# Kernel optimization log

Measured on AMD Instinct MI355X. Metric: run time of the kernel, lower is better.

The kernel has to match this reference:

```python
import jax, jax.numpy as jnp
import numpy as np

B, S, D, H, M = 2, 2048, 1024, 16, 4096  # batch, seqlen, dim, n_heads, max_seq_len
HD = D // H  # head_dim = 64
EPS = 1e-5


def layernorm(x, g, b):
    mu = jnp.mean(x, axis=-1, keepdims=True)
    var = jnp.mean((x - mu) ** 2, axis=-1, keepdims=True)
    return (x - mu) * jax.lax.rsqrt(var + EPS) * g + b


def setup_inputs() -> dict:
    key = jax.random.key(0)
    ks = jax.random.split(key, 5)
    x = jax.random.normal(ks[0], (B, S, D), jnp.float32)
    # causal mask: >=0 -> keep, negative -> drop (forward does att *= mask >= 0)
    i = jnp.arange(S)
    mask = jnp.where(i[None, :] <= i[:, None], 0, -1).astype(jnp.int32)[None, None]
    w1 = jax.random.normal(ks[1], (4 * D, D), jnp.float32) * (D ** -0.5)
    b1 = jnp.zeros((4 * D,), jnp.float32)
    w2 = jax.random.normal(ks[2], (D, D), jnp.float32) * (D ** -0.5)
    b2 = jnp.zeros((D,), jnp.float32)
    g1 = jnp.ones((D,), jnp.float32)
    beta1 = jnp.zeros((D,), jnp.float32)
    g2 = jnp.ones((D,), jnp.float32)
    beta2 = jnp.zeros((D,), jnp.float32)
    pos_w = jax.random.normal(ks[3], (2 * M - 1,), jnp.float32) * 0.02
    return dict(x=x, mask=mask, w1=w1, b1=b1, w2=w2, b2=b2,
                g1=g1, beta1=beta1, g2=g2, beta2=beta2, pos_w=pos_w)


def reference(x, mask, w1, b1, w2, b2, g1, beta1, g2, beta2, pos_w):
    # f1 + silu, split into gate u and q/k/v
    h = jax.nn.silu(x @ w1.T + b1)                      # [B,S,4D]
    u, q, k, v = jnp.split(h, 4, axis=-1)
    to_heads = lambda t: t.reshape(B, S, H, HD).transpose(0, 2, 1, 3)  # [B,H,S,HD]
    u, q, k, v = map(to_heads, (u, q, k, v))
    # relative positional bias: bias[i,j] = pos_w[M-1 + (j - i)]
    rel = jnp.arange(S)[None, :] - jnp.arange(S)[:, None]
    bias = pos_w[M - 1 + rel]                           # [S,S]
    att = jax.nn.silu(jnp.einsum('bhqd,bhkd->bhqk', q, k) + bias)
    att = att * (mask >= 0)                             # [B,H,S,S]
    y = jnp.einsum('bhqk,bhkd->bhqd', att, v) * u
    y = y.transpose(0, 2, 1, 3).reshape(B, S, D)
    y = layernorm(y, g1, beta1)
    y = y @ w2.T + b2
    return layernorm(y + x, g2, beta2)
```

## Files before the change

### kernel.cpp

```cpp
#include <hip/hip_runtime.h>
#include <hip/hip_bf16.h>

#define BN   2
#define SEQ  2048
#define DIM  1024
#define NH   16
#define HD   64
#define D4   4096
#define MAXS 4096

using bf16 = __hip_bfloat16;
typedef __bf16 bf16x8 __attribute__((ext_vector_type(8)));
typedef float  f32x4  __attribute__((ext_vector_type(4)));

__device__ __forceinline__ float bf2f(bf16 v){ return __bfloat162float(v); }
__device__ __forceinline__ bf16  f2bf(float v){ return __float2bfloat16(v); }
__device__ __forceinline__ float silu_f(float v){
  const float e = __expf(-v);
  return v * __builtin_amdgcn_rcpf(1.f + e);
}

__device__ __forceinline__ void async16(void* lds, const void* g){
  __builtin_amdgcn_global_load_lds((const __attribute__((address_space(1))) void*)g,
                                   (__attribute__((address_space(3))) void*)lds, 16, 0, 0);
}
__device__ __forceinline__ f32x4 mfma16(bf16x8 a, bf16x8 b, f32x4 c){
  return __builtin_amdgcn_mfma_f32_16x16x32_bf16(a, b, c, 0, 0, 0);
}

__global__ __launch_bounds__(256) void f2bk3(
    const float* __restrict__ a, bf16* __restrict__ ao, int na,
    const float* __restrict__ b, bf16* __restrict__ bo, int nb,
    const float* __restrict__ c, bf16* __restrict__ co)
{
  int i = (blockIdx.x * 256 + threadIdx.x) * 4;
  const float* in; bf16* out;
  if (i < na){ in = a; out = ao; }
  else if (i < na + nb){ in = b; out = bo; i -= na; }
  else { in = c; out = co; i -= na + nb; }
  const float4 v = *(const float4*)(in + i);
  bf16 t0 = f2bf(v.x), t1 = f2bf(v.y), t2 = f2bf(v.z), t3 = f2bf(v.w);
  ushort4 o;
  o.x = *(unsigned short*)&t0; o.y = *(unsigned short*)&t1;
  o.z = *(unsigned short*)&t2; o.w = *(unsigned short*)&t3;
  *(ushort4*)((unsigned short*)out + i) = o;
}

template<int NTOT>
__global__ __launch_bounds__(256) void gemm_bt(
    const bf16* __restrict__ A, const bf16* __restrict__ W,
    const float* __restrict__ bias, bf16* __restrict__ outb, bf16* __restrict__ vt)
{
  constexpr int K = DIM;
  const int ntiles = NTOT / 128;
  const int m0 = (int)(blockIdx.x / ntiles) * 128;
  const int n0 = (int)(blockIdx.x % ntiles) * 128;
  __shared__ bf16 Al[128*32];
  __shared__ bf16 Bl[128*32];
  const int tid = threadIdx.x, wave = tid>>6, lane = tid&63;
  const int quad = lane>>4, l16 = lane&15;
  const int srow = lane>>2;
  const int sg   = ((lane&3) ^ ((lane>>3)&3)) * 8;
  const int wm = (wave>>1)*64, wn = (wave&1)*64;
  const int rkey = ((l16>>1)&3);

  f32x4 acc[4][4];
  #pragma unroll
  for (int i=0;i<4;i++)
    #pragma unroll
    for (int j=0;j<4;j++) acc[i][j] = (f32x4){0.f,0.f,0.f,0.f};

  const bf16* aB = A + m0*K;
  const bf16* wB = W + n0*K;

  for (int k0 = 0; k0 < K; k0 += 32){
    async16(&Al[wave*1024      ], aB + (wave*32      + srow)*K + k0 + sg);
    async16(&Al[wave*1024 + 512], aB + (wave*32 + 16 + srow)*K + k0 + sg);
    async16(&Bl[wave*1024      ], wB + (wave*32      + srow)*K + k0 + sg);
    async16(&Bl[wave*1024 + 512], wB + (wave*32 + 16 + srow)*K + k0 + sg);
    __syncthreads();
    bf16x8 af[4], bv[4];
    #pragma unroll
    for (int mt=0;mt<4;mt++) af[mt] = *(const bf16x8*)&Al[(wm+mt*16+l16)*32 + (quad ^ rkey)*8];
    #pragma unroll
    for (int nt=0;nt<4;nt++) bv[nt] = *(const bf16x8*)&Bl[(wn+nt*16+l16)*32 + (quad ^ rkey)*8];
    #pragma unroll
    for (int mt=0;mt<4;mt++)
      #pragma unroll
      for (int nt=0;nt<4;nt++)
        acc[mt][nt] = mfma16(af[mt], bv[nt], acc[mt][nt]);
    __syncthreads();
  }

  const bool vtile = (NTOT == 4096) && (n0 >= 3*DIM);
  if (!vtile){
    #pragma unroll
    for (int mt=0;mt<4;mt++){
      #pragma unroll
      for (int nt=0;nt<4;nt++){
        const int row = m0 + wm + mt*16 + quad*4;
        const int col = n0 + wn + nt*16 + l16;
        const float bvv = bias[col];
        #pragma unroll
        for (int r=0;r<4;r++){
          float v = silu_f(acc[mt][nt][r] + bvv);
          outb[(row+r)*NTOT + col] = f2bf(v);
        }
      }
    }
  } else {
    #pragma unroll
    for (int mt=0;mt<4;mt++){
      #pragma unroll
      for (int nt=0;nt<4;nt++){
        const int row = m0 + wm + mt*16 + quad*4;
        const int colg = n0 + wn + nt*16 + l16;
        const float bvv = bias[colg];
        const int col = colg - 3*DIM;
        const int hh = col >> 6, d = col & 63;
        const int bb = row >> 11, sl = row & 2047;
        ushort4 o;
        float v0 = silu_f(acc[mt][nt][0] + bvv);
        float v1 = silu_f(acc[mt][nt][1] + bvv);
        float v2 = silu_f(acc[mt][nt][2] + bvv);
        float v3 = silu_f(acc[mt][nt][3] + bvv);
        bf16 t0=f2bf(v0), t1=f2bf(v1), t2=f2bf(v2), t3=f2bf(v3);
        o.x=*(unsigned short*)&t0; o.y=*(unsigned short*)&t1;
        o.z=*(unsigned short*)&t2; o.w=*(unsigned short*)&t3;
        *(ushort4*)&vt[((bb*NH + hh)*HD + d)*SEQ + sl] = o;
      }
    }
  }
}

__global__ __launch_bounds__(256) void gemm_bt2(
    const bf16* __restrict__ A, const bf16* __restrict__ W,
    const float* __restrict__ bias, const float* __restrict__ resid,
    float* __restrict__ outf)
{
  constexpr int K = DIM, NTOT = DIM;
  const int ntiles = NTOT / 64;
  const int m0 = (int)(blockIdx.x / ntiles) * 128;
  const int n0 = (int)(blockIdx.x % ntiles) * 64;
  __shared__ bf16 Al[128*32];
  __shared__ bf16 Bl[64*32];
  const int tid = threadIdx.x, wave = tid>>6, lane = tid&63;
  const int quad = lane>>4, l16 = lane&15;
  const int srow = lane>>2;
  const int sg   = ((lane&3) ^ ((lane>>3)&3)) * 8;
  const int wm = wave*32;
  const int rkey = ((l16>>1)&3);

  f32x4 acc[2][4];
  #pragma unroll
  for (int i=0;i<2;i++)
    #pragma unroll
    for (int j=0;j<4;j++) acc[i][j] = (f32x4){0.f,0.f,0.f,0.f};

  const bf16* aB = A + m0*K;
  const bf16* wB = W + n0*K;

  for (int k0 = 0; k0 < K; k0 += 32){
    async16(&Al[wave*1024      ], aB + (wave*32      + srow)*K + k0 + sg);
    async16(&Al[wave*1024 + 512], aB + (wave*32 + 16 + srow)*K + k0 + sg);
    async16(&Bl[wave*512       ], wB + (wave*16      + srow)*K + k0 + sg);
    __syncthreads();
    bf16x8 af[2], bv[4];
    #pragma unroll
    for (int mt=0;mt<2;mt++) af[mt] = *(const bf16x8*)&Al[(wm+mt*16+l16)*32 + (quad ^ rkey)*8];
    #pragma unroll
    for (int nt=0;nt<4;nt++) bv[nt] = *(const bf16x8*)&Bl[(nt*16+l16)*32 + (quad ^ rkey)*8];
    #pragma unroll
    for (int mt=0;mt<2;mt++)
      #pragma unroll
      for (int nt=0;nt<4;nt++)
        acc[mt][nt] = mfma16(af[mt], bv[nt], acc[mt][nt]);
    __syncthreads();
  }

  #pragma unroll
  for (int mt=0;mt<2;mt++){
    #pragma unroll
    for (int nt=0;nt<4;nt++){
      const int row = m0 + wm + mt*16 + quad*4;
      const int col = n0 + nt*16 + l16;
      const float bvv = bias[col];
      #pragma unroll
      for (int r=0;r<4;r++){
        outf[(row+r)*NTOT + col] = acc[mt][nt][r] + bvv + resid[(row+r)*NTOT + col];
      }
    }
  }
}

__global__ __launch_bounds__(256) void attn(
    const bf16* __restrict__ h, const bf16* __restrict__ vt,
    const float* __restrict__ pw, bf16* __restrict__ y)
{
  const int bid = blockIdx.x;
  const int g  = (bid & 7) + ((bid >> 7) << 3);
  const int qp = (bid >> 3) & 15;
  const int hh = g & 15, b = g >> 4;
  __shared__ bf16 Kl[128*64];
  __shared__ bf16 Vl[64*128];
  __shared__ bf16 Pl[4][16*136];
  __shared__ float pwl[256];
  const int tid = threadIdx.x, wave = tid>>6, lane = tid&63;
  const int quad = lane>>4, l16 = lane&15;

  const bf16* kgb = h + b*SEQ*D4 + 2*DIM + hh*HD;
  const bf16* vgb = vt + (b*NH + hh)*HD*SEQ;
  const int krow8 = lane>>3;
  const int kgo   = ((lane&7) ^ krow8) * 8;
  const int vrow4 = lane>>4;

  #pragma unroll
  for (int pass = 0; pass < 2; ++pass){
    const int qt = pass ? (31 - qp) : qp;
    const int q0 = qt * 64;

    const bf16* qbase = h + (b*SEQ + q0 + wave*16 + l16)*D4 + DIM + hh*HD;
    bf16x8 qf[2];
    qf[0] = *(const bf16x8*)(qbase + quad*8);
    qf[1] = *(const bf16x8*)(qbase + 32 + quad*8);

    f32x4 oacc[4];
    #pragma unroll
    for (int nt=0;nt<4;nt++) oacc[nt] = (f32x4){0.f,0.f,0.f,0.f};

    const int kmax = q0 + 64;
    for (int k0 = 0; k0 < kmax; k0 += 128){
      #pragma unroll
      for (int t=0;t<4;t++)
        async16(&Kl[(wave*32 + t*8)*64], kgb + (k0 + wave*32 + t*8 + krow8)*D4 + kgo);
      #pragma unroll
      for (int t=0;t<4;t++){
        const int vg = ((lane&15) ^ (t*4 + vrow4)) * 8;
        async16(&Vl[(wave*16 + t*4)*128], vgb + (wave*16 + t*4 + vrow4)*SEQ + k0 + vg);
      }
      const int W0 = MAXS - 1 + k0 - q0 - 63;
      if (wave == 0) async16(&pwl[0], pw + W0 + lane*4);
      __syncthreads();

      f32x4 sacc[8];
      #pragma unroll
      for (int nt=0;nt<8;nt++) sacc[nt] = (f32x4){0.f,0.f,0.f,0.f};
      #pragma unroll
      for (int ks=0;ks<2;ks++){
        #pragma unroll
        for (int nt=0;nt<8;nt++){
          bf16x8 kf = *(const bf16x8*)&Kl[(nt*16 + l16)*64 + ((ks*4 + quad) ^ (l16&7))*8];
          sacc[nt] = mfma16(kf, qf[ks], sacc[nt]);
        }
      }

      const int dq = q0 - k0;
      const int qrl = wave*16 + l16;
      #pragma unroll
      for (int nt=0;nt<8;nt++){
        const int kb = nt*16 + quad*4;
        const int d0 = kb - qrl;
        ushort4 o;
        bf16 tb[4];
        #pragma unroll
        for (int r=0;r<4;r++){
          const int d = kb + r - qrl;
          const float bias = pwl[d + 63];
          const float sv = silu_f(sacc[nt][r] + bias);
          tb[r] = f2bf((d <= dq) ? sv : 0.f);
        }
        (void)d0;
        o.x=*(unsigned short*)&tb[0]; o.y=*(unsigned short*)&tb[1];
        o.z=*(unsigned short*)&tb[2]; o.w=*(unsigned short*)&tb[3];
        *(ushort4*)&Pl[wave][l16*136 + kb] = o;
      }

      #pragma unroll
      for (int ks=0;ks<4;ks++){
        bf16x8 pf = *(const bf16x8*)&Pl[wave][l16*136 + ks*32 + quad*8];
        #pragma unroll
        for (int nt=0;nt<4;nt++){
          bf16x8 vf = *(const bf16x8*)&Vl[(nt*16 + l16)*128 + ((ks*4 + quad) ^ l16)*8];
          oacc[nt] = mfma16(pf, vf, oacc[nt]);
        }
      }
      __syncthreads();
    }

    const int qrow = q0 + wave*16 + quad*4;
    #pragma unroll
    for (int nt=0;nt<4;nt++){
      const int c = hh*HD + nt*16 + l16;
      #pragma unroll
      for (int r=0;r<4;r++){
        const int srow = b*SEQ + qrow + r;
        const float uu = bf2f(h[srow*D4 + c]);
        y[srow*DIM + c] = f2bf(oacc[nt][r] * uu);
      }
    }
    __syncthreads();
  }
}


template<bool FP32IN, bool FP32OUT>
__global__ __launch_bounds__(256) void lnorm(const void* __restrict__ in,
    const float* __restrict__ g, const float* __restrict__ be, void* __restrict__ out)
{
  const int row = blockIdx.x;
  const int tid = threadIdx.x, wave = tid>>6, lane = tid&63;
  const int c0 = tid*4;
  float v[4];
  if (FP32IN){
    const float* p = (const float*)in + row*DIM + c0;
    #pragma unroll
    for (int j=0;j<4;j++) v[j] = p[j];
  } else {
    const bf16* p = (const bf16*)in + row*DIM + c0;
    #pragma unroll
    for (int j=0;j<4;j++) v[j] = bf2f(p[j]);
  }
  float s = 0.f, ss = 0.f;
  #pragma unroll
  for (int j=0;j<4;j++){ s += v[j]; ss += v[j]*v[j]; }
  #pragma unroll
  for (int off=32; off>0; off>>=1){
    s  += __shfl_down(s, off);
    ss += __shfl_down(ss, off);
  }
  __shared__ float red[8];
  if (lane==0){ red[wave] = s; red[4+wave] = ss; }
  __syncthreads();
  s  = red[0]+red[1]+red[2]+red[3];
  ss = red[4]+red[5]+red[6]+red[7];
  const float mu   = s * (1.f/DIM);
  const float var  = ss * (1.f/DIM) - mu*mu;
  const float rstd = rsqrtf(var + 1e-5f);
  #pragma unroll
  for (int j=0;j<4;j++){
    const int c = c0 + j;
    const float o = (v[j]-mu)*rstd*g[c] + be[c];
    if (FP32OUT) ((float*)out)[row*DIM + c] = o;
    else         ((bf16*)out)[row*DIM + c] = f2bf(o);
  }
}

extern "C" void kernel_launch(void* const* d_in, const int* in_sizes, int n_in,
                              void* d_out, int out_size, void* d_ws, size_t ws_size,
                              hipStream_t stream)
{
  const float* x   = (const float*)d_in[0];
  const float* w1  = (const float*)d_in[2];
  const float* b1  = (const float*)d_in[3];
  const float* w2  = (const float*)d_in[4];
  const float* b2  = (const float*)d_in[5];
  const float* g1  = (const float*)d_in[6];
  const float* be1 = (const float*)d_in[7];
  const float* g2  = (const float*)d_in[8];
  const float* be2 = (const float*)d_in[9];
  const float* pw  = (const float*)d_in[10];

  char* ws = (char*)d_ws;
  bf16*  h   = (bf16*)(ws);
  bf16*  vt  = (bf16*)(ws + (32u<<20));
  bf16*  y   = (bf16*)(ws + (40u<<20));
  bf16*  xb  = (bf16*)(ws + (48u<<20));
  bf16*  w1b = (bf16*)(ws + (56u<<20));
  bf16*  w2b = (bf16*)(ws + (64u<<20));
  bf16*  l1  = (bf16*)(ws + (66u<<20));
  float* z   = (float*)(ws + (74u<<20));

  const int NX  = BN*SEQ*DIM;
  const int NW1 = 4*DIM*DIM;
  const int NW2 = DIM*DIM;
  f2bk3<<<dim3((NX+NW1+NW2)/1024), dim3(256), 0, stream>>>(x, xb, NX, w1, w1b, NW1, w2, w2b);

  gemm_bt<4096><<<dim3(1024), dim3(256), 0, stream>>>(xb, w1b, b1, h, vt);
  attn<<<dim3(512), dim3(256), 0, stream>>>(h, vt, pw, y);
  lnorm<false,false><<<dim3(4096), dim3(256), 0, stream>>>(y, g1, be1, l1);
  gemm_bt2<<<dim3(512), dim3(256), 0, stream>>>(l1, w2b, b2, x, z);
  lnorm<true,true><<<dim3(4096), dim3(256), 0, stream>>>(z, g2, be2, d_out);
}
```

Baseline: 244.3 us.

## Split attention KV range across two blocks and fuse u-gating into layernorm

The attention grid doubles. Each block now handles alternating 64-key chunks (an even/odd split) and writes fp32 partial outputs to two buffers, where before one block ran 128-key chunks. A new layernorm kernel sums the two partials, multiplies by the u gate and normalizes, which moves the gating out of the attention epilogue. This gives more parallelism and smaller LDS tiles for better occupancy. In exchange it writes and reads two fp32 partial arrays, adds extra global traffic and reuses workspace regions.

```diff
diff --git a/kernel.cpp b/kernel.cpp
--- a/kernel.cpp
+++ b/kernel.cpp
@@ -195,28 +195,34 @@
 
 __global__ __launch_bounds__(256) void attn(
     const bf16* __restrict__ h, const bf16* __restrict__ vt,
-    const float* __restrict__ pw, bf16* __restrict__ y)
-{
-  const int bid = blockIdx.x;
-  const int g  = (bid & 7) + ((bid >> 7) << 3);
-  const int qp = (bid >> 3) & 15;
+    const float* __restrict__ pw, float* __restrict__ yp0, float* __restrict__ yp1)
+{
+  const int bid  = blockIdx.x;
+  const int xcd  = bid & 7;
+  const int idx  = bid >> 3;
+  const int g    = ((idx >> 5) << 3) | xcd;
+  const int slot = idx & 31;
+  const int p    = slot >> 1;
+  const int ksp  = slot & 1;
   const int hh = g & 15, b = g >> 4;
-  __shared__ bf16 Kl[128*64];
-  __shared__ bf16 Vl[64*128];
-  __shared__ bf16 Pl[4][16*136];
+  float* __restrict__ yp = ksp ? yp1 : yp0;
+
+  __shared__ bf16 Kl[64*64];
+  __shared__ bf16 Vl[64*64];
+  __shared__ bf16 Pl[4][16*72];
   __shared__ float pwl[256];
+
   const int tid = threadIdx.x, wave = tid>>6, lane = tid&63;
   const int quad = lane>>4, l16 = lane&15;
+  const int r8 = lane>>3;
+  const int g8 = ((lane&7) ^ r8) * 8;
 
   const bf16* kgb = h + b*SEQ*D4 + 2*DIM + hh*HD;
   const bf16* vgb = vt + (b*NH + hh)*HD*SEQ;
-  const int krow8 = lane>>3;
-  const int kgo   = ((lane&7) ^ krow8) * 8;
-  const int vrow4 = lane>>4;
 
   #pragma unroll
   for (int pass = 0; pass < 2; ++pass){
-    const int qt = pass ? (31 - qp) : qp;
+    const int qt = pass ? (31 - p) : p;
     const int q0 = qt * 64;
 
     const bf16* qbase = h + (b*SEQ + q0 + wave*16 + l16)*D4 + DIM + hh*HD;
@@ -228,27 +234,24 @@
     #pragma unroll
     for (int nt=0;nt<4;nt++) oacc[nt] = (f32x4){0.f,0.f,0.f,0.f};
 
-    const int kmax = q0 + 64;
-    for (int k0 = 0; k0 < kmax; k0 += 128){
-      #pragma unroll
-      for (int t=0;t<4;t++)
-        async16(&Kl[(wave*32 + t*8)*64], kgb + (k0 + wave*32 + t*8 + krow8)*D4 + kgo);
-      #pragma unroll
-      for (int t=0;t<4;t++){
-        const int vg = ((lane&15) ^ (t*4 + vrow4)) * 8;
-        async16(&Vl[(wave*16 + t*4)*128], vgb + (wave*16 + t*4 + vrow4)*SEQ + k0 + vg);
-      }
-      const int W0 = MAXS - 1 + k0 - q0 - 63;
-      if (wave == 0) async16(&pwl[0], pw + W0 + lane*4);
+    for (int ic = ksp; ic <= qt; ic += 2){
+      const int k0 = ic * 64;
+      #pragma unroll
+      for (int t=0;t<2;t++)
+        async16(&Kl[(wave*16 + t*8)*64], kgb + (k0 + wave*16 + t*8 + r8)*D4 + g8);
+      #pragma unroll
+      for (int t=0;t<2;t++)
+        async16(&Vl[(wave*16 + t*8)*64], vgb + (wave*16 + t*8 + r8)*SEQ + k0 + g8);
+      if (wave == 0) async16(&pwl[0], pw + (MAXS-1 + k0 - q0 - 63) + lane*4);
       __syncthreads();
 
-      f32x4 sacc[8];
-      #pragma unroll
-      for (int nt=0;nt<8;nt++) sacc[nt] = (f32x4){0.f,0.f,0.f,0.f};
+      f32x4 sacc[4];
+      #pragma unroll
+      for (int nt=0;nt<4;nt++) sacc[nt] = (f32x4){0.f,0.f,0.f,0.f};
       #pragma unroll
       for (int ks=0;ks<2;ks++){
         #pragma unroll
-        for (int nt=0;nt<8;nt++){
+        for (int nt=0;nt<4;nt++){
           bf16x8 kf = *(const bf16x8*)&Kl[(nt*16 + l16)*64 + ((ks*4 + quad) ^ (l16&7))*8];
           sacc[nt] = mfma16(kf, qf[ks], sacc[nt]);
         }
@@ -257,10 +260,8 @@
       const int dq = q0 - k0;
       const int qrl = wave*16 + l16;
       #pragma unroll
-      for (int nt=0;nt<8;nt++){
+      for (int nt=0;nt<4;nt++){
         const int kb = nt*16 + quad*4;
-        const int d0 = kb - qrl;
-        ushort4 o;
         bf16 tb[4];
         #pragma unroll
         for (int r=0;r<4;r++){
@@ -269,18 +270,18 @@
           const float sv = silu_f(sacc[nt][r] + bias);
           tb[r] = f2bf((d <= dq) ? sv : 0.f);
         }
-        (void)d0;
+        ushort4 o;
         o.x=*(unsigned short*)&tb[0]; o.y=*(unsigned short*)&tb[1];
         o.z=*(unsigned short*)&tb[2]; o.w=*(unsigned short*)&tb[3];
-        *(ushort4*)&Pl[wave][l16*136 + kb] = o;
-      }
-
-      #pragma unroll
-      for (int ks=0;ks<4;ks++){
-        bf16x8 pf = *(const bf16x8*)&Pl[wave][l16*136 + ks*32 + quad*8];
+        *(ushort4*)&Pl[wave][l16*72 + kb] = o;
+      }
+
+      #pragma unroll
+      for (int ks=0;ks<2;ks++){
+        bf16x8 pf = *(const bf16x8*)&Pl[wave][l16*72 + ks*32 + quad*8];
         #pragma unroll
         for (int nt=0;nt<4;nt++){
-          bf16x8 vf = *(const bf16x8*)&Vl[(nt*16 + l16)*128 + ((ks*4 + quad) ^ l16)*8];
+          bf16x8 vf = *(const bf16x8*)&Vl[(nt*16 + l16)*64 + ((ks*4 + quad) ^ (l16&7))*8];
           oacc[nt] = mfma16(pf, vf, oacc[nt]);
         }
       }
@@ -293,32 +294,32 @@
       const int c = hh*HD + nt*16 + l16;
       #pragma unroll
       for (int r=0;r<4;r++){
-        const int srow = b*SEQ + qrow + r;
-        const float uu = bf2f(h[srow*D4 + c]);
-        y[srow*DIM + c] = f2bf(oacc[nt][r] * uu);
+        yp[(b*SEQ + qrow + r)*DIM + c] = oacc[nt][r];
       }
     }
-    __syncthreads();
-  }
-}
-
-
-template<bool FP32IN, bool FP32OUT>
-__global__ __launch_bounds__(256) void lnorm(const void* __restrict__ in,
-    const float* __restrict__ g, const float* __restrict__ be, void* __restrict__ out)
+  }
+}
+
+__global__ __launch_bounds__(256) void lnorm_fuse(
+    const float* __restrict__ ya, const float* __restrict__ yb,
+    const bf16* __restrict__ h, const float* __restrict__ g,
+    const float* __restrict__ be, bf16* __restrict__ out)
 {
   const int row = blockIdx.x;
   const int tid = threadIdx.x, wave = tid>>6, lane = tid&63;
   const int c0 = tid*4;
+  const float4 a  = *(const float4*)(ya + row*DIM + c0);
+  const float4 bb = *(const float4*)(yb + row*DIM + c0);
+  const ushort4 uu = *(const ushort4*)((const unsigned short*)h + row*D4 + c0);
   float v[4];
-  if (FP32IN){
-    const float* p = (const float*)in + row*DIM + c0;
-    #pragma unroll
-    for (int j=0;j<4;j++) v[j] = p[j];
-  } else {
-    const bf16* p = (const bf16*)in + row*DIM + c0;
-    #pragma unroll
-    for (int j=0;j<4;j++) v[j] = bf2f(p[j]);
+  {
+    bf16 u0,u1,u2,u3;
+    *(unsigned short*)&u0 = uu.x; *(unsigned short*)&u1 = uu.y;
+    *(unsigned short*)&u2 = uu.z; *(unsigned short*)&u3 = uu.w;
+    v[0] = (a.x + bb.x) * bf2f(u0);
+    v[1] = (a.y + bb.y) * bf2f(u1);
+    v[2] = (a.z + bb.z) * bf2f(u2);
+    v[3] = (a.w + bb.w) * bf2f(u3);
   }
   float s = 0.f, ss = 0.f;
   #pragma unroll
@@ -339,9 +340,38 @@
   #pragma unroll
   for (int j=0;j<4;j++){
     const int c = c0 + j;
-    const float o = (v[j]-mu)*rstd*g[c] + be[c];
-    if (FP32OUT) ((float*)out)[row*DIM + c] = o;
-    else         ((bf16*)out)[row*DIM + c] = f2bf(o);
+    out[row*DIM + c] = f2bf((v[j]-mu)*rstd*g[c] + be[c]);
+  }
+}
+
+__global__ __launch_bounds__(256) void lnorm2k(const float* __restrict__ in,
+    const float* __restrict__ g, const float* __restrict__ be, float* __restrict__ out)
+{
+  const int row = blockIdx.x;
+  const int tid = threadIdx.x, wave = tid>>6, lane = tid&63;
+  const int c0 = tid*4;
+  const float4 a = *(const float4*)(in + row*DIM + c0);
+  float v[4] = {a.x, a.y, a.z, a.w};
+  float s = 0.f, ss = 0.f;
+  #pragma unroll
+  for (int j=0;j<4;j++){ s += v[j]; ss += v[j]*v[j]; }
+  #pragma unroll
+  for (int off=32; off>0; off>>=1){
+    s  += __shfl_down(s, off);
+    ss += __shfl_down(ss, off);
+  }
+  __shared__ float red[8];
+  if (lane==0){ red[wave] = s; red[4+wave] = ss; }
+  __syncthreads();
+  s  = red[0]+red[1]+red[2]+red[3];
+  ss = red[4]+red[5]+red[6]+red[7];
+  const float mu   = s * (1.f/DIM);
+  const float var  = ss * (1.f/DIM) - mu*mu;
+  const float rstd = rsqrtf(var + 1e-5f);
+  #pragma unroll
+  for (int j=0;j<4;j++){
+    const int c = c0 + j;
+    out[row*DIM + c] = (v[j]-mu)*rstd*g[c] + be[c];
   }
 }
 
@@ -363,12 +393,13 @@
   char* ws = (char*)d_ws;
   bf16*  h   = (bf16*)(ws);
   bf16*  vt  = (bf16*)(ws + (32u<<20));
-  bf16*  y   = (bf16*)(ws + (40u<<20));
-  bf16*  xb  = (bf16*)(ws + (48u<<20));
-  bf16*  w1b = (bf16*)(ws + (56u<<20));
-  bf16*  w2b = (bf16*)(ws + (64u<<20));
-  bf16*  l1  = (bf16*)(ws + (66u<<20));
-  float* z   = (float*)(ws + (74u<<20));
+  float* y0  = (float*)(ws + (40u<<20));
+  float* y1  = (float*)(ws + (56u<<20));
+  bf16*  xb  = (bf16*)(ws + (72u<<20));
+  bf16*  w1b = (bf16*)(ws + (80u<<20));
+  bf16*  w2b = (bf16*)(ws + (88u<<20));
+  bf16*  l1  = (bf16*)(ws + (32u<<20));
+  float* z   = (float*)(ws + (40u<<20));
 
   const int NX  = BN*SEQ*DIM;
   const int NW1 = 4*DIM*DIM;
@@ -376,8 +407,8 @@
   f2bk3<<<dim3((NX+NW1+NW2)/1024), dim3(256), 0, stream>>>(x, xb, NX, w1, w1b, NW1, w2, w2b);
 
   gemm_bt<4096><<<dim3(1024), dim3(256), 0, stream>>>(xb, w1b, b1, h, vt);
-  attn<<<dim3(512), dim3(256), 0, stream>>>(h, vt, pw, y);
-  lnorm<false,false><<<dim3(4096), dim3(256), 0, stream>>>(y, g1, be1, l1);
+  attn<<<dim3(1024), dim3(256), 0, stream>>>(h, vt, pw, y0, y1);
+  lnorm_fuse<<<dim3(4096), dim3(256), 0, stream>>>(y0, y1, h, g1, be1, l1);
   gemm_bt2<<<dim3(512), dim3(256), 0, stream>>>(l1, w2b, b2, x, z);
-  lnorm<true,true><<<dim3(4096), dim3(256), 0, stream>>>(z, g2, be2, d_out);
-}
+  lnorm2k<<<dim3(4096), dim3(256), 0, stream>>>(z, g2, be2, (float*)d_out);
+}
```

New measurement: 246.2 us. About the same (+0.8%).

## Double GEMM K-step, swap MFMA operands for vector epilogues, split V projection

Applied to the files above, without the earlier changes.

Both GEMMs now stage 64-wide K slices in LDS with an 8-way XOR swizzle, halving the number of barrier pairs per tile. The first GEMM is split into two kernels: one for u/q/k with transposed MFMA operands so each lane writes four contiguous bf16 outputs with a float4 bias load, and one for the transposed V store. The second GEMM uses the same operand swap to get float4 residual loads and stores. The attention score MFMA operands are also swapped, which changes the P write into LDS to scalar stores. The cost is larger LDS footprint per block and an extra kernel launch.

```diff
diff --git a/kernel.cpp b/kernel.cpp
--- a/kernel.cpp
+++ b/kernel.cpp
@@ -46,23 +46,20 @@
   *(ushort4*)((unsigned short*)out + i) = o;
 }
 
-template<int NTOT>
-__global__ __launch_bounds__(256) void gemm_bt(
+__global__ __launch_bounds__(256) void gemm1_ct(
     const bf16* __restrict__ A, const bf16* __restrict__ W,
-    const float* __restrict__ bias, bf16* __restrict__ outb, bf16* __restrict__ vt)
+    const float* __restrict__ bias, bf16* __restrict__ outb)
 {
   constexpr int K = DIM;
-  const int ntiles = NTOT / 128;
-  const int m0 = (int)(blockIdx.x / ntiles) * 128;
-  const int n0 = (int)(blockIdx.x % ntiles) * 128;
-  __shared__ bf16 Al[128*32];
-  __shared__ bf16 Bl[128*32];
+  const int m0 = (int)(blockIdx.x / 24) * 128;
+  const int n0 = (int)(blockIdx.x % 24) * 128;
+  __shared__ bf16 Al[128*64];
+  __shared__ bf16 Bl[128*64];
   const int tid = threadIdx.x, wave = tid>>6, lane = tid&63;
   const int quad = lane>>4, l16 = lane&15;
-  const int srow = lane>>2;
-  const int sg   = ((lane&3) ^ ((lane>>3)&3)) * 8;
   const int wm = (wave>>1)*64, wn = (wave&1)*64;
-  const int rkey = ((l16>>1)&3);
+  const int srow = wave*8 + (lane>>3);
+  const int sg   = ((lane&7) ^ ((lane>>3)&7)) * 8;
 
   f32x4 acc[4][4];
   #pragma unroll
@@ -73,122 +70,180 @@
   const bf16* aB = A + m0*K;
   const bf16* wB = W + n0*K;
 
-  for (int k0 = 0; k0 < K; k0 += 32){
-    async16(&Al[wave*1024      ], aB + (wave*32      + srow)*K + k0 + sg);
-    async16(&Al[wave*1024 + 512], aB + (wave*32 + 16 + srow)*K + k0 + sg);
-    async16(&Bl[wave*1024      ], wB + (wave*32      + srow)*K + k0 + sg);
-    async16(&Bl[wave*1024 + 512], wB + (wave*32 + 16 + srow)*K + k0 + sg);
-    __syncthreads();
-    bf16x8 af[4], bv[4];
-    #pragma unroll
-    for (int mt=0;mt<4;mt++) af[mt] = *(const bf16x8*)&Al[(wm+mt*16+l16)*32 + (quad ^ rkey)*8];
-    #pragma unroll
-    for (int nt=0;nt<4;nt++) bv[nt] = *(const bf16x8*)&Bl[(wn+nt*16+l16)*32 + (quad ^ rkey)*8];
-    #pragma unroll
-    for (int mt=0;mt<4;mt++)
+  for (int k0 = 0; k0 < K; k0 += 64){
+    #pragma unroll
+    for (int s=0;s<4;s++){
+      async16(&Al[(s*32 + wave*8)*64], aB + (s*32 + srow)*K + k0 + sg);
+      async16(&Bl[(s*32 + wave*8)*64], wB + (s*32 + srow)*K + k0 + sg);
+    }
+    __syncthreads();
+    #pragma unroll
+    for (int ks=0;ks<2;ks++){
+      bf16x8 af[4], bv[4];
+      #pragma unroll
+      for (int mt=0;mt<4;mt++) af[mt] = *(const bf16x8*)&Al[(wm+mt*16+l16)*64 + ((ks*4+quad) ^ (l16&7))*8];
+      #pragma unroll
+      for (int nt=0;nt<4;nt++) bv[nt] = *(const bf16x8*)&Bl[(wn+nt*16+l16)*64 + ((ks*4+quad) ^ (l16&7))*8];
       #pragma unroll
       for (int nt=0;nt<4;nt++)
-        acc[mt][nt] = mfma16(af[mt], bv[nt], acc[mt][nt]);
-    __syncthreads();
-  }
-
-  const bool vtile = (NTOT == 4096) && (n0 >= 3*DIM);
-  if (!vtile){
+        #pragma unroll
+        for (int mt=0;mt<4;mt++)
+          acc[nt][mt] = mfma16(bv[nt], af[mt], acc[nt][mt]);
+    }
+    __syncthreads();
+  }
+
+  #pragma unroll
+  for (int nt=0;nt<4;nt++){
+    const int n = n0 + wn + nt*16 + quad*4;
+    const float4 b4 = *(const float4*)&bias[n];
     #pragma unroll
     for (int mt=0;mt<4;mt++){
-      #pragma unroll
-      for (int nt=0;nt<4;nt++){
-        const int row = m0 + wm + mt*16 + quad*4;
-        const int col = n0 + wn + nt*16 + l16;
-        const float bvv = bias[col];
-        #pragma unroll
-        for (int r=0;r<4;r++){
-          float v = silu_f(acc[mt][nt][r] + bvv);
-          outb[(row+r)*NTOT + col] = f2bf(v);
-        }
-      }
-    }
-  } else {
-    #pragma unroll
-    for (int mt=0;mt<4;mt++){
-      #pragma unroll
-      for (int nt=0;nt<4;nt++){
-        const int row = m0 + wm + mt*16 + quad*4;
-        const int colg = n0 + wn + nt*16 + l16;
-        const float bvv = bias[colg];
-        const int col = colg - 3*DIM;
-        const int hh = col >> 6, d = col & 63;
-        const int bb = row >> 11, sl = row & 2047;
-        ushort4 o;
-        float v0 = silu_f(acc[mt][nt][0] + bvv);
-        float v1 = silu_f(acc[mt][nt][1] + bvv);
-        float v2 = silu_f(acc[mt][nt][2] + bvv);
-        float v3 = silu_f(acc[mt][nt][3] + bvv);
-        bf16 t0=f2bf(v0), t1=f2bf(v1), t2=f2bf(v2), t3=f2bf(v3);
-        o.x=*(unsigned short*)&t0; o.y=*(unsigned short*)&t1;
-        o.z=*(unsigned short*)&t2; o.w=*(unsigned short*)&t3;
-        *(ushort4*)&vt[((bb*NH + hh)*HD + d)*SEQ + sl] = o;
-      }
-    }
-  }
-}
-
-__global__ __launch_bounds__(256) void gemm_bt2(
+      const int m = m0 + wm + mt*16 + l16;
+      bf16 t0 = f2bf(silu_f(acc[nt][mt][0] + b4.x));
+      bf16 t1 = f2bf(silu_f(acc[nt][mt][1] + b4.y));
+      bf16 t2 = f2bf(silu_f(acc[nt][mt][2] + b4.z));
+      bf16 t3 = f2bf(silu_f(acc[nt][mt][3] + b4.w));
+      ushort4 o;
+      o.x=*(unsigned short*)&t0; o.y=*(unsigned short*)&t1;
+      o.z=*(unsigned short*)&t2; o.w=*(unsigned short*)&t3;
+      *(ushort4*)&outb[m*D4 + n] = o;
+    }
+  }
+}
+
+__global__ __launch_bounds__(256) void gemm1_v(
+    const bf16* __restrict__ A, const bf16* __restrict__ W,
+    const float* __restrict__ bias, bf16* __restrict__ vt)
+{
+  constexpr int K = DIM;
+  const int m0 = (int)(blockIdx.x >> 3) * 128;
+  const int n0 = 3*DIM + (int)(blockIdx.x & 7) * 128;
+  __shared__ bf16 Al[128*64];
+  __shared__ bf16 Bl[128*64];
+  const int tid = threadIdx.x, wave = tid>>6, lane = tid&63;
+  const int quad = lane>>4, l16 = lane&15;
+  const int wm = (wave>>1)*64, wn = (wave&1)*64;
+  const int srow = wave*8 + (lane>>3);
+  const int sg   = ((lane&7) ^ ((lane>>3)&7)) * 8;
+
+  f32x4 acc[4][4];
+  #pragma unroll
+  for (int i=0;i<4;i++)
+    #pragma unroll
+    for (int j=0;j<4;j++) acc[i][j] = (f32x4){0.f,0.f,0.f,0.f};
+
+  const bf16* aB = A + m0*K;
+  const bf16* wB = W + n0*K;
+
+  for (int k0 = 0; k0 < K; k0 += 64){
+    #pragma unroll
+    for (int s=0;s<4;s++){
+      async16(&Al[(s*32 + wave*8)*64], aB + (s*32 + srow)*K + k0 + sg);
+      async16(&Bl[(s*32 + wave*8)*64], wB + (s*32 + srow)*K + k0 + sg);
+    }
+    __syncthreads();
+    #pragma unroll
+    for (int ks=0;ks<2;ks++){
+      bf16x8 af[4], bv[4];
+      #pragma unroll
+      for (int mt=0;mt<4;mt++) af[mt] = *(const bf16x8*)&Al[(wm+mt*16+l16)*64 + ((ks*4+quad) ^ (l16&7))*8];
+      #pragma unroll
+      for (int nt=0;nt<4;nt++) bv[nt] = *(const bf16x8*)&Bl[(wn+nt*16+l16)*64 + ((ks*4+quad) ^ (l16&7))*8];
+      #pragma unroll
+      for (int mt=0;mt<4;mt++)
+        #pragma unroll
+        for (int nt=0;nt<4;nt++)
+          acc[mt][nt] = mfma16(af[mt], bv[nt], acc[mt][nt]);
+    }
+    __syncthreads();
+  }
+
+  #pragma unroll
+  for (int mt=0;mt<4;mt++){
+    #pragma unroll
+    for (int nt=0;nt<4;nt++){
+      const int row = m0 + wm + mt*16 + quad*4;
+      const int colg = n0 + wn + nt*16 + l16;
+      const float bvv = bias[colg];
+      const int col = colg - 3*DIM;
+      const int hh = col >> 6, d = col & 63;
+      const int bb = row >> 11, sl = row & 2047;
+      float v0 = silu_f(acc[mt][nt][0] + bvv);
+      float v1 = silu_f(acc[mt][nt][1] + bvv);
+      float v2 = silu_f(acc[mt][nt][2] + bvv);
+      float v3 = silu_f(acc[mt][nt][3] + bvv);
+      bf16 t0=f2bf(v0), t1=f2bf(v1), t2=f2bf(v2), t3=f2bf(v3);
+      ushort4 o;
+      o.x=*(unsigned short*)&t0; o.y=*(unsigned short*)&t1;
+      o.z=*(unsigned short*)&t2; o.w=*(unsigned short*)&t3;
+      *(ushort4*)&vt[((bb*NH + hh)*HD + d)*SEQ + sl] = o;
+    }
+  }
+}
+
+__global__ __launch_bounds__(256) void gemm2_ct(
     const bf16* __restrict__ A, const bf16* __restrict__ W,
     const float* __restrict__ bias, const float* __restrict__ resid,
     float* __restrict__ outf)
 {
   constexpr int K = DIM, NTOT = DIM;
-  const int ntiles = NTOT / 64;
-  const int m0 = (int)(blockIdx.x / ntiles) * 128;
-  const int n0 = (int)(blockIdx.x % ntiles) * 64;
-  __shared__ bf16 Al[128*32];
-  __shared__ bf16 Bl[64*32];
+  const int m0 = (int)(blockIdx.x >> 4) * 128;
+  const int n0 = (int)(blockIdx.x & 15) * 64;
+  __shared__ bf16 Al[128*64];
+  __shared__ bf16 Bl[64*64];
   const int tid = threadIdx.x, wave = tid>>6, lane = tid&63;
   const int quad = lane>>4, l16 = lane&15;
-  const int srow = lane>>2;
-  const int sg   = ((lane&3) ^ ((lane>>3)&3)) * 8;
-  const int wm = wave*32;
-  const int rkey = ((l16>>1)&3);
-
-  f32x4 acc[2][4];
-  #pragma unroll
-  for (int i=0;i<2;i++)
-    #pragma unroll
-    for (int j=0;j<4;j++) acc[i][j] = (f32x4){0.f,0.f,0.f,0.f};
+  const int srow = wave*8 + (lane>>3);
+  const int sg   = ((lane&7) ^ ((lane>>3)&7)) * 8;
+
+  f32x4 acc[4][2];
+  #pragma unroll
+  for (int i=0;i<4;i++)
+    #pragma unroll
+    for (int j=0;j<2;j++) acc[i][j] = (f32x4){0.f,0.f,0.f,0.f};
 
   const bf16* aB = A + m0*K;
   const bf16* wB = W + n0*K;
 
-  for (int k0 = 0; k0 < K; k0 += 32){
-    async16(&Al[wave*1024      ], aB + (wave*32      + srow)*K + k0 + sg);
-    async16(&Al[wave*1024 + 512], aB + (wave*32 + 16 + srow)*K + k0 + sg);
-    async16(&Bl[wave*512       ], wB + (wave*16      + srow)*K + k0 + sg);
-    __syncthreads();
-    bf16x8 af[2], bv[4];
-    #pragma unroll
-    for (int mt=0;mt<2;mt++) af[mt] = *(const bf16x8*)&Al[(wm+mt*16+l16)*32 + (quad ^ rkey)*8];
-    #pragma unroll
-    for (int nt=0;nt<4;nt++) bv[nt] = *(const bf16x8*)&Bl[(nt*16+l16)*32 + (quad ^ rkey)*8];
-    #pragma unroll
-    for (int mt=0;mt<2;mt++)
+  for (int k0 = 0; k0 < K; k0 += 64){
+    #pragma unroll
+    for (int s=0;s<4;s++)
+      async16(&Al[(s*32 + wave*8)*64], aB + (s*32 + srow)*K + k0 + sg);
+    #pragma unroll
+    for (int s=0;s<2;s++)
+      async16(&Bl[(s*32 + wave*8)*64], wB + (s*32 + srow)*K + k0 + sg);
+    __syncthreads();
+    #pragma unroll
+    for (int ks=0;ks<2;ks++){
+      bf16x8 af[2], bv[4];
+      #pragma unroll
+      for (int mt=0;mt<2;mt++) af[mt] = *(const bf16x8*)&Al[(wave*32+mt*16+l16)*64 + ((ks*4+quad) ^ (l16&7))*8];
+      #pragma unroll
+      for (int nt=0;nt<4;nt++) bv[nt] = *(const bf16x8*)&Bl[(nt*16+l16)*64 + ((ks*4+quad) ^ (l16&7))*8];
       #pragma unroll
       for (int nt=0;nt<4;nt++)
-        acc[mt][nt] = mfma16(af[mt], bv[nt], acc[mt][nt]);
-    __syncthreads();
-  }
-
-  #pragma unroll
-  for (int mt=0;mt<2;mt++){
-    #pragma unroll
-    for (int nt=0;nt<4;nt++){
-      const int row = m0 + wm + mt*16 + quad*4;
-      const int col = n0 + nt*16 + l16;
-      const float bvv = bias[col];
-      #pragma unroll
-      for (int r=0;r<4;r++){
-        outf[(row+r)*NTOT + col] = acc[mt][nt][r] + bvv + resid[(row+r)*NTOT + col];
-      }
+        #pragma unroll
+        for (int mt=0;mt<2;mt++)
+          acc[nt][mt] = mfma16(bv[nt], af[mt], acc[nt][mt]);
+    }
+    __syncthreads();
+  }
+
+  #pragma unroll
+  for (int nt=0;nt<4;nt++){
+    const int n = n0 + nt*16 + quad*4;
+    const float4 b4 = *(const float4*)&bias[n];
+    #pragma unroll
+    for (int mt=0;mt<2;mt++){
+      const int m = m0 + wave*32 + mt*16 + l16;
+      const float4 r4 = *(const float4*)&resid[m*NTOT + n];
+      float4 o;
+      o.x = acc[nt][mt][0] + b4.x + r4.x;
+      o.y = acc[nt][mt][1] + b4.y + r4.y;
+      o.z = acc[nt][mt][2] + b4.z + r4.z;
+      o.w = acc[nt][mt][3] + b4.w + r4.w;
+      *(float4*)&outf[m*NTOT + n] = o;
     }
   }
 }
@@ -250,29 +305,21 @@
         #pragma unroll
         for (int nt=0;nt<8;nt++){
           bf16x8 kf = *(const bf16x8*)&Kl[(nt*16 + l16)*64 + ((ks*4 + quad) ^ (l16&7))*8];
-          sacc[nt] = mfma16(kf, qf[ks], sacc[nt]);
+          sacc[nt] = mfma16(qf[ks], kf, sacc[nt]);
         }
       }
-
+      const int li = wave*16 + quad*4;
       const int dq = q0 - k0;
-      const int qrl = wave*16 + l16;
       #pragma unroll
       for (int nt=0;nt<8;nt++){
-        const int kb = nt*16 + quad*4;
-        const int d0 = kb - qrl;
-        ushort4 o;
-        bf16 tb[4];
+        const int lj = nt*16 + l16;
         #pragma unroll
         for (int r=0;r<4;r++){
-          const int d = kb + r - qrl;
-          const float bias = pwl[d + 63];
+          const float bias = pwl[lj - (li+r) + 63];
           const float sv = silu_f(sacc[nt][r] + bias);
-          tb[r] = f2bf((d <= dq) ? sv : 0.f);
+          const float v = (lj - (li+r) <= dq) ? sv : 0.f;
+          Pl[wave][(quad*4+r)*136 + lj] = f2bf(v);
         }
-        (void)d0;
-        o.x=*(unsigned short*)&tb[0]; o.y=*(unsigned short*)&tb[1];
-        o.z=*(unsigned short*)&tb[2]; o.w=*(unsigned short*)&tb[3];
-        *(ushort4*)&Pl[wave][l16*136 + kb] = o;
       }
 
       #pragma unroll
@@ -301,7 +348,6 @@
     __syncthreads();
   }
 }
-
 
 template<bool FP32IN, bool FP32OUT>
 __global__ __launch_bounds__(256) void lnorm(const void* __restrict__ in,
@@ -375,9 +421,10 @@
   const int NW2 = DIM*DIM;
   f2bk3<<<dim3((NX+NW1+NW2)/1024), dim3(256), 0, stream>>>(x, xb, NX, w1, w1b, NW1, w2, w2b);
 
-  gemm_bt<4096><<<dim3(1024), dim3(256), 0, stream>>>(xb, w1b, b1, h, vt);
+  gemm1_ct<<<dim3(768), dim3(256), 0, stream>>>(xb, w1b, b1, h);
+  gemm1_v <<<dim3(256), dim3(256), 0, stream>>>(xb, w1b, b1, vt);
   attn<<<dim3(512), dim3(256), 0, stream>>>(h, vt, pw, y);
   lnorm<false,false><<<dim3(4096), dim3(256), 0, stream>>>(y, g1, be1, l1);
-  gemm_bt2<<<dim3(512), dim3(256), 0, stream>>>(l1, w2b, b2, x, z);
+  gemm2_ct<<<dim3(512), dim3(256), 0, stream>>>(l1, w2b, b2, x, z);
   lnorm<true,true><<<dim3(4096), dim3(256), 0, stream>>>(z, g2, be2, d_out);
 }
```

Result: slower. 256.1 us (+4.8%).
